# Kernel tuning notes

Hardware: AMD Instinct MI355X
Metric: run time of the kernel (lower is better)

Reference implementation:

```python
import jax, jax.numpy as jnp
import numpy as np

B, L, H, N, COND = 32, 32768, 32, 16, 4
N2 = N // 2  # S4D stores N/2 complex conjugate-pair modes


def setup_inputs() -> dict:
    key = jax.random.key(0)
    ks = jax.random.split(key, 8)
    x = jax.random.normal(ks[0], (B, L, H), jnp.float32)
    cond = jax.random.normal(ks[1], (B, COND), jnp.float32)
    # S4D kernel parameters (state-spaces minimal S4D init)
    log_dt = np.log(1e-3) + jax.random.uniform(ks[2], (H,), jnp.float32) * (np.log(1e-1) - np.log(1e-3))
    C_re = jax.random.normal(ks[3], (H, N2), jnp.float32) * (0.5 ** 0.5)
    C_im = jax.random.normal(ks[4], (H, N2), jnp.float32) * (0.5 ** 0.5)
    log_A_real = jnp.log(0.5 * jnp.ones((H, N2), jnp.float32))
    A_imag = jnp.pi * jnp.tile(jnp.arange(N2, dtype=jnp.float32), (H, 1))
    D = jax.random.normal(ks[5], (H,), jnp.float32)
    # FiLM linear: cond -> (gamma, beta)
    film_W = jax.random.normal(ks[6], (COND, 2 * H), jnp.float32) / np.sqrt(COND)
    film_b = jnp.zeros((2 * H,), jnp.float32)
    return dict(x=x, cond=cond, log_dt=log_dt, C_re=C_re, C_im=C_im,
                log_A_real=log_A_real, A_imag=A_imag, D=D,
                film_W=film_W, film_b=film_b)


def reference(x, cond, log_dt, C_re, C_im, log_A_real, A_imag, D, film_W, film_b):
    # x: (B, L, H) -> DSSM over channel-major layout (B, H, L)
    u = jnp.transpose(x, (0, 2, 1))  # B H L
    # --- S4D kernel: K[h, l] = 2 * Re( sum_n C~_hn * exp(dt_h * A_hn * l) )
    dt = jnp.exp(log_dt)[:, None]                      # (H, 1)
    A = -jnp.exp(log_A_real) + 1j * A_imag             # (H, N2) complex
    dtA = A * dt                                       # (H, N2)
    Ct = (C_re + 1j * C_im) * (jnp.exp(dtA) - 1.0) / A # discretized C
    vand = jnp.exp(dtA[:, :, None] * jnp.arange(L, dtype=jnp.float32))  # (H, N2, L)
    K = 2.0 * jnp.einsum('hn,hnl->hl', Ct, vand).real  # (H, L)
    # --- causal convolution via FFT on length-2L circular pad
    n_fft = 2 * L
    y = jnp.fft.irfft(jnp.fft.rfft(u, n=n_fft) * jnp.fft.rfft(K, n=n_fft), n=n_fft)[..., :L]
    y = y + u * D[:, None]                             # skip connection
    y = jnp.transpose(y, (0, 2, 1))                    # back to (B, L, H)
    # --- FiLM conditioning
    gb = cond @ film_W + film_b                        # (B, 2H)
    gamma, beta = gb[:, :H], gb[:, H:]
    y = gamma[:, None, :] * y + beta[:, None, :]
    # --- activation
    return jax.nn.gelu(y)
```

## Files before the change

kernel.cpp:

```cpp
#include <hip/hip_runtime.h>

typedef float v2f __attribute__((ext_vector_type(2)));

#define BB 32
#define LL 32768
#define HH 32
#define NN2 8
#define NCOND 4
#define NCHUNK 256
#define LC (LL / NCHUNK)

#define PARAM_OFF 0
#define WLC_OFF   1024
#define FILM_OFF  1536
#define S_OFF     4096
#define SZ_S      (BB * HH * NCHUNK * 16)

static __device__ __forceinline__ v2f vfma(v2f a, v2f b, v2f c) {
  return __builtin_elementwise_fma(a, b, c);
}

__global__ void setup_kernel(const float* __restrict__ log_dt,
                             const float* __restrict__ C_re,
                             const float* __restrict__ C_im,
                             const float* __restrict__ log_A_real,
                             const float* __restrict__ A_imag,
                             const float* __restrict__ cond,
                             const float* __restrict__ film_W,
                             const float* __restrict__ film_b,
                             float* __restrict__ ws) {
  int idx = blockIdx.x * blockDim.x + threadIdx.x;
  if (idx < HH * NN2) {
    int h = idx >> 3, n = idx & (NN2 - 1);
    float dt = expf(log_dt[h]);
    float ar = -expf(log_A_real[idx]);
    float ai = A_imag[idx];
    float dr = ar * dt, di = ai * dt;
    float er = expf(dr);
    float wr = er * cosf(di);
    float wi = er * sinf(di);
    float den = ar * ar + ai * ai;
    float tr = ((wr - 1.f) * ar + wi * ai) / den;
    float ti = (wi * ar - (wr - 1.f) * ai) / den;
    float cr = C_re[idx], ci = C_im[idx];
    float ctr = 2.f * (cr * tr - ci * ti);
    float cti = 2.f * (cr * ti + ci * tr);
    float* p = ws + PARAM_OFF + h * 32;
    p[n] = wr; p[n + 8] = wi; p[n + 16] = ctr; p[n + 24] = cti;
    float eL  = expf(dr * (float)LC);
    float wlr = eL * cosf(di * (float)LC);
    float wli = eL * sinf(di * (float)LC);
    float* q = ws + WLC_OFF + idx * 2;
    q[0] = wlr; q[1] = wli;
  }
  int f = idx - HH * NN2;
  if (f >= 0 && f < BB * HH) {
    int b = f >> 5, h = f & (HH - 1);
    float g  = film_b[h];
    float be = film_b[h + HH];
    #pragma unroll
    for (int c2 = 0; c2 < NCOND; c2++) {
      float cv = cond[b * NCOND + c2];
      g  = fmaf(cv, film_W[c2 * 2 * HH + h], g);
      be = fmaf(cv, film_W[c2 * 2 * HH + HH + h], be);
    }
    float* p = ws + FILM_OFF + f * 2;
    p[0] = g; p[1] = be;
  }
}

__global__ __launch_bounds__(256) void pass_a(const float* __restrict__ x,
                                              float* __restrict__ ws) {
  const int flat = blockIdx.x * 256 + threadIdx.x;
  const int h = flat & (HH - 1);
  const int c = (flat >> 5) & (NCHUNK - 1);
  const int b = flat >> 13;
  const v2f* pp = (const v2f*)(ws + PARAM_OFF + h * 32);
  v2f wr[4], wi[4], zr[4], zi[4];
  #pragma unroll
  for (int g = 0; g < 4; g++) {
    wr[g] = pp[g]; wi[g] = pp[4 + g];
    zr[g] = (v2f){0.f, 0.f}; zi[g] = (v2f){0.f, 0.f};
  }
  const float* xp = x + ((size_t)b * LL + (size_t)c * LC) * HH + h;
  for (int i = 0; i < LC; i += 8) {
    float u[8];
    #pragma unroll
    for (int j = 0; j < 8; j++) u[j] = xp[(size_t)(i + j) * HH];
    #pragma unroll
    for (int j = 0; j < 8; j++) {
      v2f us = (v2f){u[j], u[j]};
      #pragma unroll
      for (int g = 0; g < 4; g++) {
        v2f t0  = vfma(-wi[g], zi[g], us);
        v2f nzr = vfma(wr[g], zr[g], t0);
        v2f nzi = vfma(wr[g], zi[g], wi[g] * zr[g]);
        zr[g] = nzr; zi[g] = nzi;
      }
    }
  }
  v2f* Sp = (v2f*)(ws + S_OFF + (size_t)flat * 16);
  #pragma unroll
  for (int g = 0; g < 4; g++) { Sp[g] = zr[g]; Sp[4 + g] = zi[g]; }
}

__global__ __launch_bounds__(256) void pass_b(float* __restrict__ ws) {
  const int bh = blockIdx.x;
  const int b  = bh >> 5;
  const int h  = bh & (HH - 1);
  const int t  = threadIdx.x;

  __shared__ __align__(16) float Lbuf[NCHUNK][18];

  float* Sp = ws + S_OFF +
              ((size_t)b * (NCHUNK * HH) + (size_t)t * HH + h) * 16;

  v2f zr[4], zi[4];
  #pragma unroll
  for (int g = 0; g < 4; g++) {
    zr[g] = ((const v2f*)Sp)[g];
    zi[g] = ((const v2f*)Sp)[4 + g];
  }

  const float* q = ws + WLC_OFF + h * NN2 * 2;
  v2f mr[4], mi[4];
  #pragma unroll
  for (int g = 0; g < 4; g++) {
    mr[g] = (v2f){q[4 * g + 0], q[4 * g + 2]};
    mi[g] = (v2f){q[4 * g + 1], q[4 * g + 3]};
  }

  v2f* rowv = (v2f*)&Lbuf[t][0];
  #pragma unroll
  for (int g = 0; g < 4; g++) { rowv[g] = zr[g]; rowv[4 + g] = zi[g]; }
  __syncthreads();

  #pragma unroll
  for (int d = 1; d < NCHUNK; d <<= 1) {
    v2f ar[4], ai[4];
    #pragma unroll
    for (int g = 0; g < 4; g++) { ar[g] = (v2f){0.f, 0.f}; ai[g] = (v2f){0.f, 0.f}; }
    if (t >= d) {
      const v2f* prow = (const v2f*)&Lbuf[t - d][0];
      #pragma unroll
      for (int g = 0; g < 4; g++) { ar[g] = prow[g]; ai[g] = prow[4 + g]; }
    }
    __syncthreads();
    #pragma unroll
    for (int g = 0; g < 4; g++) {
      zr[g] = vfma(mr[g], ar[g], vfma(-mi[g], ai[g], zr[g]));
      zi[g] = vfma(mr[g], ai[g], vfma(mi[g], ar[g], zi[g]));
      rowv[g] = zr[g]; rowv[4 + g] = zi[g];
      v2f nmr = vfma(mr[g], mr[g], -(mi[g] * mi[g]));
      v2f nmi = (mr[g] + mr[g]) * mi[g];
      mr[g] = nmr; mi[g] = nmi;
    }
    __syncthreads();
  }

  v2f er[4], ei[4];
  #pragma unroll
  for (int g = 0; g < 4; g++) { er[g] = (v2f){0.f, 0.f}; ei[g] = (v2f){0.f, 0.f}; }
  if (t > 0) {
    const v2f* prow = (const v2f*)&Lbuf[t - 1][0];
    #pragma unroll
    for (int g = 0; g < 4; g++) { er[g] = prow[g]; ei[g] = prow[4 + g]; }
  }
  #pragma unroll
  for (int g = 0; g < 4; g++) {
    ((v2f*)Sp)[g] = er[g];
    ((v2f*)Sp)[4 + g] = ei[g];
  }
}

__global__ __launch_bounds__(256) void pass_c(const float* __restrict__ x,
                                              const float* __restrict__ Dv,
                                              float* __restrict__ out,
                                              float* __restrict__ ws) {
  const int flat = blockIdx.x * 256 + threadIdx.x;
  const int h = flat & (HH - 1);
  const int c = (flat >> 5) & (NCHUNK - 1);
  const int b = flat >> 13;
  const v2f* pp = (const v2f*)(ws + PARAM_OFF + h * 32);
  v2f wr[4], wi[4], ctr[4], cti[4], zr[4], zi[4];
  #pragma unroll
  for (int g = 0; g < 4; g++) {
    wr[g] = pp[g]; wi[g] = pp[4 + g]; ctr[g] = pp[8 + g]; cti[g] = pp[12 + g];
  }
  const v2f* Zp = (const v2f*)(ws + S_OFF + (size_t)flat * 16);
  #pragma unroll
  for (int g = 0; g < 4; g++) { zr[g] = Zp[g]; zi[g] = Zp[4 + g]; }
  float gamma = ws[FILM_OFF + ((size_t)b * HH + h) * 2];
  float beta  = ws[FILM_OFF + ((size_t)b * HH + h) * 2 + 1];
  float dcoef = Dv[h];
  const size_t off = ((size_t)b * LL + (size_t)c * LC) * HH + h;
  const float* xp = x + off;
  float* op = out + off;
  for (int i = 0; i < LC; i += 8) {
    float u[8];
    #pragma unroll
    for (int j = 0; j < 8; j++) u[j] = xp[(size_t)(i + j) * HH];
    #pragma unroll
    for (int j = 0; j < 8; j++) {
      v2f us = (v2f){u[j], u[j]};
      v2f acc = (v2f){0.f, 0.f};
      #pragma unroll
      for (int g = 0; g < 4; g++) {
        v2f t0  = vfma(-wi[g], zi[g], us);
        v2f nzr = vfma(wr[g], zr[g], t0);
        v2f nzi = vfma(wr[g], zi[g], wi[g] * zr[g]);
        zr[g] = nzr; zi[g] = nzi;
        acc = vfma(ctr[g], nzr, acc);
        acc = vfma(-cti[g], nzi, acc);
      }
      float y = acc.x + acc.y;
      y = fmaf(dcoef, u[j], y);
      y = fmaf(gamma, y, beta);
      float y3   = y * y * y;
      float targ = 0.7978845608f * fmaf(0.044715f, y3, y);
      float e    = __expf(2.f * targ);
      float th   = 1.f - __fdividef(2.f, e + 1.f);
      __builtin_nontemporal_store(0.5f * y * (1.f + th),
                                  op + (size_t)(i + j) * HH);
    }
  }
}

extern "C" void kernel_launch(void* const* d_in, const int* in_sizes, int n_in,
                              void* d_out, int out_size, void* d_ws, size_t ws_size,
                              hipStream_t stream) {
  const float* x          = (const float*)d_in[0];
  const float* cond       = (const float*)d_in[1];
  const float* log_dt     = (const float*)d_in[2];
  const float* C_re       = (const float*)d_in[3];
  const float* C_im       = (const float*)d_in[4];
  const float* log_A_real = (const float*)d_in[5];
  const float* A_imag     = (const float*)d_in[6];
  const float* Dv         = (const float*)d_in[7];
  const float* film_W     = (const float*)d_in[8];
  const float* film_b     = (const float*)d_in[9];
  float* out = (float*)d_out;
  float* ws  = (float*)d_ws;

  setup_kernel<<<5, 256, 0, stream>>>(log_dt, C_re, C_im, log_A_real, A_imag,
                                      cond, film_W, film_b, ws);
  pass_a<<<(BB * HH * NCHUNK) / 256, 256, 0, stream>>>(x, ws);
  pass_b<<<BB * HH, 256, 0, stream>>>(ws);
  pass_c<<<(BB * HH * NCHUNK) / 256, 256, 0, stream>>>(x, Dv, out, ws);
}
```

Before: 307.3 us.

## Split SSM modes across two lanes and software-prefetch inputs in scan passes

Each (batch, chunk, channel) scan is now split across two threads that each own half of the eight complex modes, doubling thread count in pass_a and pass_c. In pass_c the two halves' partial outputs are combined with a cross-half wavefront shuffle, and each lane writes alternate timesteps. Input loads are also double-buffered so the next eight samples are fetched while the current ones are processed. This shortens each thread's serial recurrence and raises occupancy, but every x element is now loaded twice and pass_c adds shuffles and select logic.

New measurement: 310.8 us. Within noise of the previous version (+1.1%).

```diff
diff --git a/kernel.cpp b/kernel.cpp
--- a/kernel.cpp
+++ b/kernel.cpp
@@ -72,36 +72,47 @@
 __global__ __launch_bounds__(256) void pass_a(const float* __restrict__ x,
                                               float* __restrict__ ws) {
   const int flat = blockIdx.x * 256 + threadIdx.x;
-  const int h = flat & (HH - 1);
-  const int c = (flat >> 5) & (NCHUNK - 1);
-  const int b = flat >> 13;
+  const int h  = flat & (HH - 1);
+  const int nh = (flat >> 5) & 1;
+  const int c  = (flat >> 6) & (NCHUNK - 1);
+  const int b  = flat >> 14;
   const v2f* pp = (const v2f*)(ws + PARAM_OFF + h * 32);
-  v2f wr[4], wi[4], zr[4], zi[4];
-  #pragma unroll
-  for (int g = 0; g < 4; g++) {
-    wr[g] = pp[g]; wi[g] = pp[4 + g];
+  v2f wr[2], wi[2], zr[2], zi[2];
+  #pragma unroll
+  for (int g = 0; g < 2; g++) {
+    wr[g] = pp[nh * 2 + g]; wi[g] = pp[4 + nh * 2 + g];
     zr[g] = (v2f){0.f, 0.f}; zi[g] = (v2f){0.f, 0.f};
   }
   const float* xp = x + ((size_t)b * LL + (size_t)c * LC) * HH + h;
+  float u[8], un[8];
+  #pragma unroll
+  for (int j = 0; j < 8; j++) u[j] = xp[(size_t)j * HH];
+  #pragma unroll 2
   for (int i = 0; i < LC; i += 8) {
-    float u[8];
-    #pragma unroll
-    for (int j = 0; j < 8; j++) u[j] = xp[(size_t)(i + j) * HH];
+    const int ip = (i + 8 < LC) ? (i + 8) : i;
+    #pragma unroll
+    for (int j = 0; j < 8; j++) un[j] = xp[(size_t)(ip + j) * HH];
     #pragma unroll
     for (int j = 0; j < 8; j++) {
       v2f us = (v2f){u[j], u[j]};
       #pragma unroll
-      for (int g = 0; g < 4; g++) {
+      for (int g = 0; g < 2; g++) {
         v2f t0  = vfma(-wi[g], zi[g], us);
         v2f nzr = vfma(wr[g], zr[g], t0);
         v2f nzi = vfma(wr[g], zi[g], wi[g] * zr[g]);
         zr[g] = nzr; zi[g] = nzi;
       }
     }
-  }
-  v2f* Sp = (v2f*)(ws + S_OFF + (size_t)flat * 16);
-  #pragma unroll
-  for (int g = 0; g < 4; g++) { Sp[g] = zr[g]; Sp[4 + g] = zi[g]; }
+    #pragma unroll
+    for (int j = 0; j < 8; j++) u[j] = un[j];
+  }
+  const size_t flatbch = ((size_t)b * NCHUNK + c) * HH + h;
+  v2f* Sp = (v2f*)(ws + S_OFF + flatbch * 16);
+  #pragma unroll
+  for (int g = 0; g < 2; g++) {
+    Sp[nh * 2 + g]     = zr[g];
+    Sp[4 + nh * 2 + g] = zi[g];
+  }
 }
 
 __global__ __launch_bounds__(256) void pass_b(float* __restrict__ ws) {
@@ -178,51 +189,79 @@
                                               float* __restrict__ out,
                                               float* __restrict__ ws) {
   const int flat = blockIdx.x * 256 + threadIdx.x;
-  const int h = flat & (HH - 1);
-  const int c = (flat >> 5) & (NCHUNK - 1);
-  const int b = flat >> 13;
+  const int h  = flat & (HH - 1);
+  const int nh = (flat >> 5) & 1;
+  const int c  = (flat >> 6) & (NCHUNK - 1);
+  const int b  = flat >> 14;
   const v2f* pp = (const v2f*)(ws + PARAM_OFF + h * 32);
-  v2f wr[4], wi[4], ctr[4], cti[4], zr[4], zi[4];
-  #pragma unroll
-  for (int g = 0; g < 4; g++) {
-    wr[g] = pp[g]; wi[g] = pp[4 + g]; ctr[g] = pp[8 + g]; cti[g] = pp[12 + g];
-  }
-  const v2f* Zp = (const v2f*)(ws + S_OFF + (size_t)flat * 16);
-  #pragma unroll
-  for (int g = 0; g < 4; g++) { zr[g] = Zp[g]; zi[g] = Zp[4 + g]; }
+  v2f wr[2], wi[2], ctr[2], cti[2], zr[2], zi[2];
+  #pragma unroll
+  for (int g = 0; g < 2; g++) {
+    wr[g]  = pp[nh * 2 + g];      wi[g]  = pp[4 + nh * 2 + g];
+    ctr[g] = pp[8 + nh * 2 + g];  cti[g] = pp[12 + nh * 2 + g];
+  }
+  const size_t flatbch = ((size_t)b * NCHUNK + c) * HH + h;
+  const v2f* Zp = (const v2f*)(ws + S_OFF + flatbch * 16);
+  #pragma unroll
+  for (int g = 0; g < 2; g++) {
+    zr[g] = Zp[nh * 2 + g];
+    zi[g] = Zp[4 + nh * 2 + g];
+  }
   float gamma = ws[FILM_OFF + ((size_t)b * HH + h) * 2];
   float beta  = ws[FILM_OFF + ((size_t)b * HH + h) * 2 + 1];
   float dcoef = Dv[h];
   const size_t off = ((size_t)b * LL + (size_t)c * LC) * HH + h;
   const float* xp = x + off;
   float* op = out + off;
+  float u[8], un[8];
+  #pragma unroll
+  for (int j = 0; j < 8; j++) u[j] = xp[(size_t)j * HH];
+  #pragma unroll 2
   for (int i = 0; i < LC; i += 8) {
-    float u[8];
-    #pragma unroll
-    for (int j = 0; j < 8; j++) u[j] = xp[(size_t)(i + j) * HH];
-    #pragma unroll
-    for (int j = 0; j < 8; j++) {
-      v2f us = (v2f){u[j], u[j]};
-      v2f acc = (v2f){0.f, 0.f};
-      #pragma unroll
-      for (int g = 0; g < 4; g++) {
-        v2f t0  = vfma(-wi[g], zi[g], us);
+    const int ip = (i + 8 < LC) ? (i + 8) : i;
+    #pragma unroll
+    for (int j = 0; j < 8; j++) un[j] = xp[(size_t)(ip + j) * HH];
+    #pragma unroll
+    for (int j = 0; j < 8; j += 2) {
+      v2f us0 = (v2f){u[j], u[j]};
+      v2f acc0 = (v2f){0.f, 0.f};
+      #pragma unroll
+      for (int g = 0; g < 2; g++) {
+        v2f t0  = vfma(-wi[g], zi[g], us0);
         v2f nzr = vfma(wr[g], zr[g], t0);
         v2f nzi = vfma(wr[g], zi[g], wi[g] * zr[g]);
         zr[g] = nzr; zi[g] = nzi;
-        acc = vfma(ctr[g], nzr, acc);
-        acc = vfma(-cti[g], nzi, acc);
+        acc0 = vfma(ctr[g], nzr, acc0);
+        acc0 = vfma(-cti[g], nzi, acc0);
       }
-      float y = acc.x + acc.y;
-      y = fmaf(dcoef, u[j], y);
+      v2f us1 = (v2f){u[j + 1], u[j + 1]};
+      v2f acc1 = (v2f){0.f, 0.f};
+      #pragma unroll
+      for (int g = 0; g < 2; g++) {
+        v2f t0  = vfma(-wi[g], zi[g], us1);
+        v2f nzr = vfma(wr[g], zr[g], t0);
+        v2f nzi = vfma(wr[g], zi[g], wi[g] * zr[g]);
+        zr[g] = nzr; zi[g] = nzi;
+        acc1 = vfma(ctr[g], nzr, acc1);
+        acc1 = vfma(-cti[g], nzi, acc1);
+      }
+      float y0 = acc0.x + acc0.y;
+      float y1 = acc1.x + acc1.y;
+      y0 += __shfl_xor(y0, 32, 64);
+      y1 += __shfl_xor(y1, 32, 64);
+      float ysel = nh ? y1 : y0;
+      float usel = nh ? u[j + 1] : u[j];
+      float y = fmaf(dcoef, usel, ysel);
       y = fmaf(gamma, y, beta);
       float y3   = y * y * y;
       float targ = 0.7978845608f * fmaf(0.044715f, y3, y);
       float e    = __expf(2.f * targ);
       float th   = 1.f - __fdividef(2.f, e + 1.f);
       __builtin_nontemporal_store(0.5f * y * (1.f + th),
-                                  op + (size_t)(i + j) * HH);
-    }
+                                  op + (size_t)(i + j + nh) * HH);
+    }
+    #pragma unroll
+    for (int j = 0; j < 8; j++) u[j] = un[j];
   }
 }
 
@@ -244,7 +283,7 @@
 
   setup_kernel<<<5, 256, 0, stream>>>(log_dt, C_re, C_im, log_A_real, A_imag,
                                       cond, film_W, film_b, ws);
-  pass_a<<<(BB * HH * NCHUNK) / 256, 256, 0, stream>>>(x, ws);
+  pass_a<<<(BB * HH * NCHUNK * 2) / 256, 256, 0, stream>>>(x, ws);
   pass_b<<<BB * HH, 256, 0, stream>>>(ws);
-  pass_c<<<(BB * HH * NCHUNK) / 256, 256, 0, stream>>>(x, Dv, out, ws);
-}
+  pass_c<<<(BB * HH * NCHUNK * 2) / 256, 256, 0, stream>>>(x, Dv, out, ws);
+}
```

## Split SSM modes across lane pairs with paired-channel vector loads and shuffle reduction

Applied to the files above, without the earlier changes.

Pass A and pass C now give each thread two adjacent channels and half of the modes. Threads 16 apart handle the other half, and their partial outputs are combined with a cross-lane shuffle. Loads become 8-byte float2 reads with one-step register prefetch, and the recurrences use inline-asm v_pk_fma/v_pk_mul. GELU is rewritten as a sigmoid form with one exp per element. This halves the serial per-thread recurrence work so more threads can hide latency, at the cost of shuffle overhead, a duplicated recurrence over both channel pairs, and inline asm that limits compiler scheduling.

After: 339.7 us. 10.6% more time.

```diff
diff --git a/kernel.cpp b/kernel.cpp
--- a/kernel.cpp
+++ b/kernel.cpp
@@ -14,10 +14,20 @@
 #define WLC_OFF   1024
 #define FILM_OFF  1536
 #define S_OFF     4096
-#define SZ_S      (BB * HH * NCHUNK * 16)
 
 static __device__ __forceinline__ v2f vfma(v2f a, v2f b, v2f c) {
   return __builtin_elementwise_fma(a, b, c);
+}
+
+static __device__ __forceinline__ v2f pk_fma(v2f a, v2f b, v2f c) {
+  v2f d;
+  asm("v_pk_fma_f32 %0, %1, %2, %3" : "=v"(d) : "v"(a), "v"(b), "v"(c));
+  return d;
+}
+static __device__ __forceinline__ v2f pk_mul(v2f a, v2f b) {
+  v2f d;
+  asm("v_pk_mul_f32 %0, %1, %2" : "=v"(d) : "v"(a), "v"(b));
+  return d;
 }
 
 __global__ void setup_kernel(const float* __restrict__ log_dt,
@@ -72,36 +82,62 @@
 __global__ __launch_bounds__(256) void pass_a(const float* __restrict__ x,
                                               float* __restrict__ ws) {
   const int flat = blockIdx.x * 256 + threadIdx.x;
-  const int h = flat & (HH - 1);
-  const int c = (flat >> 5) & (NCHUNK - 1);
-  const int b = flat >> 13;
-  const v2f* pp = (const v2f*)(ws + PARAM_OFF + h * 32);
-  v2f wr[4], wi[4], zr[4], zi[4];
-  #pragma unroll
-  for (int g = 0; g < 4; g++) {
-    wr[g] = pp[g]; wi[g] = pp[4 + g];
-    zr[g] = (v2f){0.f, 0.f}; zi[g] = (v2f){0.f, 0.f};
-  }
-  const float* xp = x + ((size_t)b * LL + (size_t)c * LC) * HH + h;
-  for (int i = 0; i < LC; i += 8) {
-    float u[8];
-    #pragma unroll
-    for (int j = 0; j < 8; j++) u[j] = xp[(size_t)(i + j) * HH];
-    #pragma unroll
-    for (int j = 0; j < 8; j++) {
-      v2f us = (v2f){u[j], u[j]};
+  const int h2 = flat & 15;
+  const int nh = (flat >> 4) & 1;
+  const int c  = (flat >> 5) & (NCHUNK - 1);
+  const int b  = flat >> 13;
+  const int h0 = h2 << 1;
+
+  v2f wr[2][2], wi[2][2], nwi[2][2], zr[2][2], zi[2][2];
+  #pragma unroll
+  for (int hh = 0; hh < 2; hh++) {
+    const v2f* pp = (const v2f*)(ws + PARAM_OFF + (h0 + hh) * 32);
+    #pragma unroll
+    for (int g = 0; g < 2; g++) {
+      wr[hh][g] = pp[nh * 2 + g]; wi[hh][g] = pp[4 + nh * 2 + g];
+      nwi[hh][g] = (v2f){-wi[hh][g].x, -wi[hh][g].y};
+      zr[hh][g] = (v2f){0.f, 0.f}; zi[hh][g] = (v2f){0.f, 0.f};
+    }
+  }
+  const float* xp = x + ((size_t)b * LL + (size_t)c * LC) * HH + h0;
+  v2f u[4], un[4];
+  #pragma unroll
+  for (int j = 0; j < 4; j++) u[j] = *(const v2f*)(xp + (size_t)j * HH);
+  for (int i = 0; i < LC; i += 4) {
+    const int ip = (i + 4 < LC) ? (i + 4) : i;
+    #pragma unroll
+    for (int j = 0; j < 4; j++) un[j] = *(const v2f*)(xp + (size_t)(ip + j) * HH);
+    #pragma unroll
+    for (int j = 0; j < 4; j++) {
+      v2f us0 = (v2f){u[j].x, u[j].x};
+      v2f us1 = (v2f){u[j].y, u[j].y};
       #pragma unroll
-      for (int g = 0; g < 4; g++) {
-        v2f t0  = vfma(-wi[g], zi[g], us);
-        v2f nzr = vfma(wr[g], zr[g], t0);
-        v2f nzi = vfma(wr[g], zi[g], wi[g] * zr[g]);
-        zr[g] = nzr; zi[g] = nzi;
+      for (int g = 0; g < 2; g++) {
+        v2f t0  = pk_fma(nwi[0][g], zi[0][g], us0);
+        v2f nzr = pk_fma(wr[0][g], zr[0][g], t0);
+        v2f t1  = pk_mul(wi[0][g], zr[0][g]);
+        zi[0][g] = pk_fma(wr[0][g], zi[0][g], t1);
+        zr[0][g] = nzr;
+        v2f s0  = pk_fma(nwi[1][g], zi[1][g], us1);
+        v2f mzr = pk_fma(wr[1][g], zr[1][g], s0);
+        v2f s1  = pk_mul(wi[1][g], zr[1][g]);
+        zi[1][g] = pk_fma(wr[1][g], zi[1][g], s1);
+        zr[1][g] = mzr;
       }
     }
-  }
-  v2f* Sp = (v2f*)(ws + S_OFF + (size_t)flat * 16);
-  #pragma unroll
-  for (int g = 0; g < 4; g++) { Sp[g] = zr[g]; Sp[4 + g] = zi[g]; }
+    #pragma unroll
+    for (int j = 0; j < 4; j++) u[j] = un[j];
+  }
+  #pragma unroll
+  for (int hh = 0; hh < 2; hh++) {
+    const size_t flatbch = ((size_t)b * NCHUNK + c) * HH + h0 + hh;
+    v2f* Sp = (v2f*)(ws + S_OFF + flatbch * 16);
+    #pragma unroll
+    for (int g = 0; g < 2; g++) {
+      Sp[nh * 2 + g]     = zr[hh][g];
+      Sp[4 + nh * 2 + g] = zi[hh][g];
+    }
+  }
 }
 
 __global__ __launch_bounds__(256) void pass_b(float* __restrict__ ws) {
@@ -178,51 +214,98 @@
                                               float* __restrict__ out,
                                               float* __restrict__ ws) {
   const int flat = blockIdx.x * 256 + threadIdx.x;
-  const int h = flat & (HH - 1);
-  const int c = (flat >> 5) & (NCHUNK - 1);
-  const int b = flat >> 13;
-  const v2f* pp = (const v2f*)(ws + PARAM_OFF + h * 32);
-  v2f wr[4], wi[4], ctr[4], cti[4], zr[4], zi[4];
-  #pragma unroll
-  for (int g = 0; g < 4; g++) {
-    wr[g] = pp[g]; wi[g] = pp[4 + g]; ctr[g] = pp[8 + g]; cti[g] = pp[12 + g];
-  }
-  const v2f* Zp = (const v2f*)(ws + S_OFF + (size_t)flat * 16);
-  #pragma unroll
-  for (int g = 0; g < 4; g++) { zr[g] = Zp[g]; zi[g] = Zp[4 + g]; }
-  float gamma = ws[FILM_OFF + ((size_t)b * HH + h) * 2];
-  float beta  = ws[FILM_OFF + ((size_t)b * HH + h) * 2 + 1];
-  float dcoef = Dv[h];
-  const size_t off = ((size_t)b * LL + (size_t)c * LC) * HH + h;
+  const int h2 = flat & 15;
+  const int nh = (flat >> 4) & 1;
+  const int c  = (flat >> 5) & (NCHUNK - 1);
+  const int b  = flat >> 13;
+  const int h0 = h2 << 1;
+
+  v2f wr[2][2], wi[2][2], nwi[2][2], ctr[2][2], ncti[2][2], zr[2][2], zi[2][2];
+  #pragma unroll
+  for (int hh = 0; hh < 2; hh++) {
+    const v2f* pp = (const v2f*)(ws + PARAM_OFF + (h0 + hh) * 32);
+    #pragma unroll
+    for (int g = 0; g < 2; g++) {
+      wr[hh][g]  = pp[nh * 2 + g];      wi[hh][g]  = pp[4 + nh * 2 + g];
+      nwi[hh][g] = (v2f){-wi[hh][g].x, -wi[hh][g].y};
+      ctr[hh][g] = pp[8 + nh * 2 + g];
+      v2f ct = pp[12 + nh * 2 + g];
+      ncti[hh][g] = (v2f){-ct.x, -ct.y};
+    }
+    const size_t flatbch = ((size_t)b * NCHUNK + c) * HH + h0 + hh;
+    const v2f* Zp = (const v2f*)(ws + S_OFF + flatbch * 16);
+    #pragma unroll
+    for (int g = 0; g < 2; g++) {
+      zr[hh][g] = Zp[nh * 2 + g];
+      zi[hh][g] = Zp[4 + nh * 2 + g];
+    }
+  }
+  v2f gam, bet, dco;
+  {
+    const float* fp = ws + FILM_OFF + ((size_t)b * HH + h0) * 2;
+    gam = (v2f){fp[0], fp[2]};
+    bet = (v2f){fp[1], fp[3]};
+    dco = (v2f){Dv[h0], Dv[h0 + 1]};
+  }
+  const size_t off = ((size_t)b * LL + (size_t)c * LC) * HH + h0;
   const float* xp = x + off;
   float* op = out + off;
-  for (int i = 0; i < LC; i += 8) {
-    float u[8];
-    #pragma unroll
-    for (int j = 0; j < 8; j++) u[j] = xp[(size_t)(i + j) * HH];
-    #pragma unroll
-    for (int j = 0; j < 8; j++) {
-      v2f us = (v2f){u[j], u[j]};
-      v2f acc = (v2f){0.f, 0.f};
+  v2f u[4], un[4];
+  #pragma unroll
+  for (int j = 0; j < 4; j++) u[j] = *(const v2f*)(xp + (size_t)j * HH);
+  for (int i = 0; i < LC; i += 4) {
+    const int ip = (i + 4 < LC) ? (i + 4) : i;
+    #pragma unroll
+    for (int j = 0; j < 4; j++) un[j] = *(const v2f*)(xp + (size_t)(ip + j) * HH);
+    #pragma unroll
+    for (int j = 0; j < 4; j += 2) {
+      v2f yv[2];
       #pragma unroll
-      for (int g = 0; g < 4; g++) {
-        v2f t0  = vfma(-wi[g], zi[g], us);
-        v2f nzr = vfma(wr[g], zr[g], t0);
-        v2f nzi = vfma(wr[g], zi[g], wi[g] * zr[g]);
-        zr[g] = nzr; zi[g] = nzi;
-        acc = vfma(ctr[g], nzr, acc);
-        acc = vfma(-cti[g], nzi, acc);
+      for (int e = 0; e < 2; e++) {
+        v2f uu = u[j + e];
+        v2f us0 = (v2f){uu.x, uu.x};
+        v2f us1 = (v2f){uu.y, uu.y};
+        v2f a0 = (v2f){0.f, 0.f}, a1 = (v2f){0.f, 0.f};
+        #pragma unroll
+        for (int g = 0; g < 2; g++) {
+          v2f t0  = pk_fma(nwi[0][g], zi[0][g], us0);
+          v2f nzr = pk_fma(wr[0][g], zr[0][g], t0);
+          v2f t1  = pk_mul(wi[0][g], zr[0][g]);
+          zi[0][g] = pk_fma(wr[0][g], zi[0][g], t1);
+          zr[0][g] = nzr;
+          a0 = pk_fma(ctr[0][g], zr[0][g], a0);
+          a0 = pk_fma(ncti[0][g], zi[0][g], a0);
+          v2f s0  = pk_fma(nwi[1][g], zi[1][g], us1);
+          v2f mzr = pk_fma(wr[1][g], zr[1][g], s0);
+          v2f s1  = pk_mul(wi[1][g], zr[1][g]);
+          zi[1][g] = pk_fma(wr[1][g], zi[1][g], s1);
+          zr[1][g] = mzr;
+          a1 = pk_fma(ctr[1][g], zr[1][g], a1);
+          a1 = pk_fma(ncti[1][g], zi[1][g], a1);
+        }
+        yv[e] = (v2f){a0.x + a0.y, a1.x + a1.y};
       }
-      float y = acc.x + acc.y;
-      y = fmaf(dcoef, u[j], y);
-      y = fmaf(gamma, y, beta);
-      float y3   = y * y * y;
-      float targ = 0.7978845608f * fmaf(0.044715f, y3, y);
-      float e    = __expf(2.f * targ);
-      float th   = 1.f - __fdividef(2.f, e + 1.f);
-      __builtin_nontemporal_store(0.5f * y * (1.f + th),
-                                  op + (size_t)(i + j) * HH);
-    }
+      #pragma unroll
+      for (int e = 0; e < 2; e++) {
+        yv[e].x += __shfl_xor(yv[e].x, 16, 64);
+        yv[e].y += __shfl_xor(yv[e].y, 16, 64);
+      }
+      v2f ysel = nh ? yv[1] : yv[0];
+      v2f usel = nh ? u[j + 1] : u[j];
+      v2f y = vfma(dco, usel, ysel);
+      y = vfma(gam, y, bet);
+      v2f y2 = y * y;
+      v2f s  = y * vfma((v2f){0.0713548755f, 0.0713548755f}, y2,
+                        (v2f){1.5957691216f, 1.5957691216f});
+      float e0 = __expf(-s.x);
+      float e1 = __expf(-s.y);
+      float r0 = __fdividef(y.x, 1.f + e0);
+      float r1 = __fdividef(y.y, 1.f + e1);
+      v2f res = (v2f){r0, r1};
+      __builtin_nontemporal_store(res, (v2f*)(op + (size_t)(i + j + nh) * HH));
+    }
+    #pragma unroll
+    for (int j = 0; j < 4; j++) u[j] = un[j];
   }
 }
 
```

## Double chunk count, prefetch inputs in scan passes, simplify GELU

Applied to the files above, without the earlier changes.

Doubles the number of sequence chunks from 256 to 512. This halves the serial recurrence length per thread and doubles the threads in passes A and C, with pass B's block scan widened to 512 threads. Both scan passes now software-prefetch the next 8 inputs while computing the current ones, to hide global-load latency. The tanh-form GELU is rewritten as y*sigmoid(s), saving a few instructions. The cost is a deeper cross-chunk scan with more barriers and a larger state buffer.

Result: slower. 317.7 us (+3.4%).

```diff
diff --git a/kernel.cpp b/kernel.cpp
--- a/kernel.cpp
+++ b/kernel.cpp
@@ -7,14 +7,13 @@
 #define HH 32
 #define NN2 8
 #define NCOND 4
-#define NCHUNK 256
+#define NCHUNK 512
 #define LC (LL / NCHUNK)
 
 #define PARAM_OFF 0
 #define WLC_OFF   1024
 #define FILM_OFF  1536
 #define S_OFF     4096
-#define SZ_S      (BB * HH * NCHUNK * 16)
 
 static __device__ __forceinline__ v2f vfma(v2f a, v2f b, v2f c) {
   return __builtin_elementwise_fma(a, b, c);
@@ -74,7 +73,7 @@
   const int flat = blockIdx.x * 256 + threadIdx.x;
   const int h = flat & (HH - 1);
   const int c = (flat >> 5) & (NCHUNK - 1);
-  const int b = flat >> 13;
+  const int b = flat >> 14;
   const v2f* pp = (const v2f*)(ws + PARAM_OFF + h * 32);
   v2f wr[4], wi[4], zr[4], zi[4];
   #pragma unroll
@@ -83,10 +82,13 @@
     zr[g] = (v2f){0.f, 0.f}; zi[g] = (v2f){0.f, 0.f};
   }
   const float* xp = x + ((size_t)b * LL + (size_t)c * LC) * HH + h;
+  float u[8], un[8];
+  #pragma unroll
+  for (int j = 0; j < 8; j++) u[j] = xp[(size_t)j * HH];
   for (int i = 0; i < LC; i += 8) {
-    float u[8];
-    #pragma unroll
-    for (int j = 0; j < 8; j++) u[j] = xp[(size_t)(i + j) * HH];
+    const int ip = (i + 8 < LC) ? (i + 8) : i;
+    #pragma unroll
+    for (int j = 0; j < 8; j++) un[j] = xp[(size_t)(ip + j) * HH];
     #pragma unroll
     for (int j = 0; j < 8; j++) {
       v2f us = (v2f){u[j], u[j]};
@@ -98,13 +100,15 @@
         zr[g] = nzr; zi[g] = nzi;
       }
     }
+    #pragma unroll
+    for (int j = 0; j < 8; j++) u[j] = un[j];
   }
   v2f* Sp = (v2f*)(ws + S_OFF + (size_t)flat * 16);
   #pragma unroll
   for (int g = 0; g < 4; g++) { Sp[g] = zr[g]; Sp[4 + g] = zi[g]; }
 }
 
-__global__ __launch_bounds__(256) void pass_b(float* __restrict__ ws) {
+__global__ __launch_bounds__(512) void pass_b(float* __restrict__ ws) {
   const int bh = blockIdx.x;
   const int b  = bh >> 5;
   const int h  = bh & (HH - 1);
@@ -180,7 +184,7 @@
   const int flat = blockIdx.x * 256 + threadIdx.x;
   const int h = flat & (HH - 1);
   const int c = (flat >> 5) & (NCHUNK - 1);
-  const int b = flat >> 13;
+  const int b = flat >> 14;
   const v2f* pp = (const v2f*)(ws + PARAM_OFF + h * 32);
   v2f wr[4], wi[4], ctr[4], cti[4], zr[4], zi[4];
   #pragma unroll
@@ -196,10 +200,13 @@
   const size_t off = ((size_t)b * LL + (size_t)c * LC) * HH + h;
   const float* xp = x + off;
   float* op = out + off;
+  float u[8], un[8];
+  #pragma unroll
+  for (int j = 0; j < 8; j++) u[j] = xp[(size_t)j * HH];
   for (int i = 0; i < LC; i += 8) {
-    float u[8];
-    #pragma unroll
-    for (int j = 0; j < 8; j++) u[j] = xp[(size_t)(i + j) * HH];
+    const int ip = (i + 8 < LC) ? (i + 8) : i;
+    #pragma unroll
+    for (int j = 0; j < 8; j++) un[j] = xp[(size_t)(ip + j) * HH];
     #pragma unroll
     for (int j = 0; j < 8; j++) {
       v2f us = (v2f){u[j], u[j]};
@@ -216,13 +223,14 @@
       float y = acc.x + acc.y;
       y = fmaf(dcoef, u[j], y);
       y = fmaf(gamma, y, beta);
-      float y3   = y * y * y;
-      float targ = 0.7978845608f * fmaf(0.044715f, y3, y);
-      float e    = __expf(2.f * targ);
-      float th   = 1.f - __fdividef(2.f, e + 1.f);
-      __builtin_nontemporal_store(0.5f * y * (1.f + th),
-                                  op + (size_t)(i + j) * HH);
-    }
+      float y2 = y * y;
+      float s  = y * fmaf(0.0713548755f, y2, 1.5957691216f);
+      float ex = __expf(-s);
+      float r  = __fdividef(y, 1.f + ex);
+      __builtin_nontemporal_store(r, op + (size_t)(i + j) * HH);
+    }
+    #pragma unroll
+    for (int j = 0; j < 8; j++) u[j] = un[j];
   }
 }
 
@@ -245,6 +253,6 @@
   setup_kernel<<<5, 256, 0, stream>>>(log_dt, C_re, C_im, log_A_real, A_imag,
                                       cond, film_W, film_b, ws);
   pass_a<<<(BB * HH * NCHUNK) / 256, 256, 0, stream>>>(x, ws);
-  pass_b<<<BB * HH, 256, 0, stream>>>(ws);
+  pass_b<<<BB * HH, 512, 0, stream>>>(ws);
   pass_c<<<(BB * HH * NCHUNK) / 256, 256, 0, stream>>>(x, Dv, out, ws);
 }
```
